# Kernel optimization log

Hardware: AMD Instinct MI355X
Metric: run time of the kernel (lower is better)

Reference implementation:

```python
import jax, jax.numpy as jnp
import numpy as np

# ---- static config (mirrors init_kwargs) ----
H, N, HKV = 32, 64, 8
HN = H * N            # model dim 2048
KV_DIM = HKV * N      # 512
B, T = 2, 1024
EPS = 1e-6
ROPE_THETA = 1.0e6
SPLITS_WAVGK = (96, 96, 64, 256, 64)   # xw, xa, xv, xg, xk lora ranks
SPLITS_RKV = (HN, KV_DIM, KV_DIM)


def rms_norm(x, w, eps=EPS):
    xf = x.astype(jnp.float32)
    var = jnp.mean(xf * xf, axis=-1, keepdims=True)
    return (w * (xf * jax.lax.rsqrt(var + eps))).astype(x.dtype)


def rotate_half(x):
    x1, x2 = jnp.split(x, 2, axis=-1)
    return jnp.concatenate((-x2, x1), axis=-1)


def apply_rope(q, k, cos, sin):
    # q:[B,T,H,N], k:[B,T,HKV,N], cos/sin:[B,T,N] -> unsqueeze head dim (unsqueeze_dim=2)
    cos = cos[:, :, None, :]
    sin = sin[:, :, None, :]
    return q * cos + rotate_half(q) * sin, k * cos + rotate_half(k) * sin


def rwkv7_recurrence(r, gk, k, v, a, b, S0):
    # fused_recurrent_rwkv7 (head_first=False). All inputs [B,T,H,N] fp32, S0 [B,H,N_key,N_val].
    # S_t = diag(exp(gk_t)) S_{t-1} + b_t (a_t^T S_{t-1}) + k_t v_t^T ;  o_t = r_t^T S_t
    def step(S, inp):
        r_t, w_t, k_t, v_t, a_t, b_t = inp
        sa = jnp.einsum('bhk,bhkv->bhv', a_t, S)
        S = (jnp.exp(w_t)[..., None] * S
             + k_t[..., None] * v_t[..., None, :]
             + b_t[..., None] * sa[..., None, :])
        o = jnp.einsum('bhk,bhkv->bhv', r_t, S)
        return S, o
    xs = tuple(jnp.swapaxes(t, 0, 1) for t in (r, gk, k, v, a, b))  # [T,B,H,N]
    S, o = jax.lax.scan(step, S0, xs)
    return jnp.swapaxes(o, 0, 1), S


def setup_inputs() -> dict:
    key = jax.random.key(0)
    ks = jax.random.split(key, 24)
    f32 = jnp.float32
    rn = lambda k, shape, s=1.0: jax.random.normal(k, shape, dtype=f32) * s

    x_in = rn(ks[0], (B, T, HN))
    v_first = rn(ks[1], (B, T, HKV, N))
    k_first = rn(ks[2], (B, T, HKV, N))
    state = jnp.zeros((B, H, N, N), f32)

    # real rope cache (faithful to get_batch_rope_cache output) at positions 0..T-1
    inv_freq = 1.0 / (ROPE_THETA ** (np.arange(0, N, 2, dtype=np.float32) / N))
    freqs = np.outer(np.arange(T, dtype=np.float32), inv_freq)  # [T, N/2]
    emb = np.concatenate([freqs, freqs], axis=-1)               # [T, N]
    calc_cos = jnp.broadcast_to(jnp.asarray(np.cos(emb), dtype=np.float32), (B, T, N))
    calc_sin = jnp.broadcast_to(jnp.asarray(np.sin(emb), dtype=np.float32), (B, T, N))

    wavgk1 = rn(ks[3], (HN, sum(SPLITS_WAVGK)), 0.02)
    w0 = rn(ks[4], (HN,), 0.5)
    w2 = rn(ks[5], (SPLITS_WAVGK[0], HN), 0.02)
    a0 = rn(ks[6], (HN,), 0.1)
    a2 = rn(ks[7], (SPLITS_WAVGK[1], HN), 0.02)
    v0 = rn(ks[8], (KV_DIM,), 0.1)
    v2 = rn(ks[9], (SPLITS_WAVGK[2], KV_DIM), 0.02)
    g2 = rn(ks[10], (SPLITS_WAVGK[3], HN), 0.02)
    k0 = rn(ks[11], (KV_DIM,), 0.1)
    k2 = rn(ks[12], (SPLITS_WAVGK[4], KV_DIM), 0.02)
    r_k = rn(ks[13], (H, N), 0.1)
    RKV = rn(ks[14], (HN, HN + 2 * KV_DIM), 0.02)   # fpx weight, dequantized form
    O = rn(ks[15], (HN, HN), 0.02)
    R_bias = rn(ks[16], (HN,), 0.02)
    K_bias = rn(ks[17], (KV_DIM,), 0.02)
    V_bias = rn(ks[18], (KV_DIM,), 0.02)
    ln_r = jnp.ones((N,), f32)
    ln_k = jnp.ones((N,), f32)
    ln1 = jnp.ones((HN,), f32)
    ln2 = jnp.ones((HN,), f32)

    return dict(x_in=x_in, v_first=v_first, k_first=k_first, state=state,
                calc_cos=calc_cos, calc_sin=calc_sin, wavgk1=wavgk1,
                w0=w0, w2=w2, a0=a0, a2=a2, v0=v0, v2=v2, g2=g2, k0=k0, k2=k2,
                r_k=r_k, RKV=RKV, O=O, R_bias=R_bias, K_bias=K_bias, V_bias=V_bias,
                ln_r=ln_r, ln_k=ln_k, ln1=ln1, ln2=ln2)


def reference(x_in, v_first, k_first, state, calc_cos, calc_sin, wavgk1,
              w0, w2, a0, a2, v0, v2, g2, k0, k2, r_k, RKV, O,
              R_bias, K_bias, V_bias, ln_r, ln_k, ln1, ln2):
    Bx, Tx, C = x_in.shape
    kv_repeat = HN // KV_DIM  # GQA repeat factor (4)

    x = rms_norm(x_in, ln1)
    xw, xa, xv, xg, xk = jnp.split(x @ wavgk1, np.cumsum(SPLITS_WAVGK)[:-1].tolist(), axis=-1)

    rkv = x @ RKV  # fpx_matmul -> dense matmul on dequantized weight
    r, k, v = jnp.split(rkv, np.cumsum(SPLITS_RKV)[:-1].tolist(), axis=-1)
    r = (r + R_bias).reshape(Bx, Tx, H, N)
    k = (k + K_bias).reshape(Bx, Tx, HKV, N)
    v = (v + V_bias).reshape(Bx, Tx, HKV, N)

    r = rms_norm(r, ln_r)
    k = rms_norm(k, ln_k)
    r, k = apply_rope(r, k, calc_cos, calc_sin)

    # layer_id = 1 (> 0): mix with first-layer value/key
    v = v + (v_first - v) * jax.nn.sigmoid(xv @ v2 + v0).reshape(Bx, Tx, HKV, N)
    k = k + (k_first - k) * jax.nn.sigmoid(xk @ k2 + k0).reshape(Bx, Tx, HKV, N)

    # repeat_kv: [B,T,HKV,N] -> [B,T,H,N] -> [B,T,HN]
    k = jnp.repeat(k, kv_repeat, axis=2).reshape(Bx, Tx, HN)
    v = jnp.repeat(v, kv_repeat, axis=2).reshape(Bx, Tx, HN)

    a = jax.nn.sigmoid(xa @ a2 + a0)  # in-context learning rate gate [B,T,HN]
    k4 = k.reshape(Bx, Tx, H, N)
    kk = (k4 / jnp.maximum(jnp.linalg.norm(k4, axis=-1, keepdims=True), 1e-12)).reshape(Bx, Tx, HN)

    w_log = -jax.nn.softplus(-(jnp.tanh(xw) @ w2 + w0)) - 0.5  # log-decay, <= -0.5
    k = k * (1.0 - w_log + a)
    aa = -kk
    bb = kk * a
    gk = -jnp.exp(w_log.astype(jnp.float32))  # passed to fused_recurrent_rwkv7 as log decay

    shp = (Bx, Tx, H, N)
    o, state_out = rwkv7_recurrence(
        r.reshape(shp).astype(jnp.float32), gk.reshape(shp),
        k.reshape(shp).astype(jnp.float32), v.reshape(shp).astype(jnp.float32),
        aa.reshape(shp).astype(jnp.float32), bb.reshape(shp).astype(jnp.float32),
        state.astype(jnp.float32))

    xx = o.reshape(Bx, Tx, HN) * (float(N) ** -0.5)
    bonus = ((r * k.reshape(shp) * r_k).sum(axis=-1, keepdims=True) * v.reshape(shp)).reshape(Bx, Tx, HN)
    xx = xx.astype(x_in.dtype) + bonus

    out = (xx * (jax.nn.sigmoid(xg) @ g2)) @ O  # fpx output projection
    x_new = x_in + out
    return rms_norm(x_new, ln2)
```

## Files before the change

kernel.cpp:

```cpp
#include <hip/hip_runtime.h>

typedef unsigned short u16;
typedef unsigned int u32;

using f32x4 = __attribute__((ext_vector_type(4))) float;
using bf16x8 = __attribute__((ext_vector_type(8))) __bf16;

#define HN 2048
#define KVD 512
#define TOKENS 2048
#define N1 3712
#define K2W 576
#define N2 7168

#define OFF_Y1   0ull
#define OFF_OO   0ull
#define OFF_XG   16777216ull
#define OFF_Y2   30408704ull
#define OFF_OUTR 60817408ull
#define OFF_BT1  89128960ull
#define OFF_XB   104333312ull
#define OFF_W2T  89128960ull
#define OFF_X2   97386496ull
#define OFF_OT   89128960ull
#define OFF_DEC  129499136ull
#define OFF_VV   163053568ull
#define OFF_PAB  213385216ull
#define OFF_PKR  230162432ull
#define OFF_DOT  246939648ull
#define WS_NEED  247201792ull

__device__ __forceinline__ u16 f2bf(float f) {
    u32 u = __float_as_uint(f);
    u32 r = u + 0x7fffu + ((u >> 16) & 1u);
    return (u16)(r >> 16);
}
__device__ __forceinline__ float bf2f(u16 b) {
    return __uint_as_float(((u32)b) << 16);
}
__device__ __forceinline__ float sigm(float x) { return 1.f / (1.f + expf(-x)); }
__device__ __forceinline__ float wsum(float v) {
#pragma unroll
    for (int m = 32; m > 0; m >>= 1) v += __shfl_xor(v, m, 64);
    return v;
}
__device__ __forceinline__ float rowsum16(float v) {
    float t;
    t = __uint_as_float(__builtin_amdgcn_update_dpp(0, __float_as_uint(v), 0x121, 0xf, 0xf, true));
    v += t;
    t = __uint_as_float(__builtin_amdgcn_update_dpp(0, __float_as_uint(v), 0x122, 0xf, 0xf, true));
    v += t;
    t = __uint_as_float(__builtin_amdgcn_update_dpp(0, __float_as_uint(v), 0x124, 0xf, 0xf, true));
    v += t;
    t = __uint_as_float(__builtin_amdgcn_update_dpp(0, __float_as_uint(v), 0x128, 0xf, 0xf, true));
    v += t;
    return v;
}

typedef __attribute__((address_space(1))) const void glob_t;
typedef __attribute__((address_space(3))) void lds_t;
__device__ __forceinline__ void gload_lds16(const void* g, void* l) {
    __builtin_amdgcn_global_load_lds((glob_t*)g, (lds_t*)l, 16, 0, 0);
}

template<int OFF>
__device__ __forceinline__ float4 ds_read128(u32 a) {
    float4 r;
    asm volatile("ds_read_b128 %0, %1 offset:%2" : "=v"(r) : "v"(a), "i"(OFF));
    return r;
}
template<int OFF>
__device__ __forceinline__ uint4 ds_read128u(u32 a) {
    uint4 r;
    asm volatile("ds_read_b128 %0, %1 offset:%2" : "=v"(r) : "v"(a), "i"(OFF));
    return r;
}
template<int OFF>
__device__ __forceinline__ float ds_read32(u32 a) {
    float r;
    asm volatile("ds_read_b32 %0, %1 offset:%2" : "=v"(r) : "v"(a), "i"(OFF));
    return r;
}

__global__ __launch_bounds__(256) void k_prep_bt1(const float* __restrict__ wavgk1,
                                                  const float* __restrict__ RKV,
                                                  u16* __restrict__ BT1) {
    __shared__ float tile[64][65];
    const int bn = blockIdx.x >> 5;
    const int bk = blockIdx.x & 31;
    const int n0 = bn << 6, k0 = bk << 6;
    const int c = threadIdx.x & 63, q = threadIdx.x >> 6;
#pragma unroll
    for (int i = 0; i < 16; ++i) {
        const int r = (q << 4) + i;
        float v = 0.f;
        if (bn < 9)       v = wavgk1[(size_t)(k0 + r) * 576 + n0 + c];
        else if (bn < 57) v = RKV[(size_t)(k0 + r) * 3072 + (n0 + c - 576)];
        tile[r][c] = v;
    }
    __syncthreads();
#pragma unroll
    for (int i = 0; i < 16; ++i) {
        const int rw = (q << 4) + i;
        BT1[(size_t)(n0 + rw) * 2048 + k0 + c] = f2bf(tile[c][rw]);
    }
}

__global__ __launch_bounds__(256) void k_prep_w2t(const float* __restrict__ w2, const float* __restrict__ a2,
                                                  const float* __restrict__ g2, const float* __restrict__ v2,
                                                  const float* __restrict__ k2, u16* __restrict__ W2T) {
    __shared__ float tile[64][65];
    const int bx = blockIdx.x;
    const int bn = bx / 9, bc = bx - bn * 9;
    const int n0 = bn << 6, c0 = bc << 6;
    const int cc = threadIdx.x & 63, q = threadIdx.x >> 6;
#pragma unroll
    for (int i = 0; i < 16; ++i) {
        const int r = (q << 4) + i;
        const int c = c0 + r;
        const int n = n0 + cc;
        float v = 0.f;
        if (n0 < 2048)      { if (c < 96)              v = w2[(size_t)c * 2048 + n]; }
        else if (n0 < 4096) { if (c >= 96 && c < 192)  v = a2[(size_t)(c - 96) * 2048 + (n - 2048)]; }
        else if (n0 < 6144) { if (c >= 192 && c < 448) v = g2[(size_t)(c - 192) * 2048 + (n - 4096)]; }
        else if (n0 < 6656) { if (c >= 448 && c < 512) v = v2[(size_t)(c - 448) * 512 + (n - 6144)]; }
        else                { if (c >= 512)            v = k2[(size_t)(c - 512) * 512 + (n - 6656)]; }
        tile[r][cc] = v;
    }
    __syncthreads();
#pragma unroll
    for (int i = 0; i < 16; ++i) {
        const int rw = (q << 4) + i;
        W2T[(size_t)(n0 + rw) * 576 + c0 + cc] = f2bf(tile[cc][rw]);
    }
}

__global__ __launch_bounds__(256) void k_prep_ot(const float* __restrict__ O, u16* __restrict__ OT) {
    __shared__ float tile[64][65];
    const int bn = blockIdx.x >> 5, bk = blockIdx.x & 31;
    const int n0 = bn << 6, k0 = bk << 6;
    const int c = threadIdx.x & 63, q = threadIdx.x >> 6;
#pragma unroll
    for (int i = 0; i < 16; ++i) {
        const int r = (q << 4) + i;
        tile[r][c] = O[(size_t)(k0 + r) * 2048 + n0 + c];
    }
    __syncthreads();
#pragma unroll
    for (int i = 0; i < 16; ++i) {
        const int rw = (q << 4) + i;
        OT[(size_t)(n0 + rw) * 2048 + k0 + c] = f2bf(tile[c][rw]);
    }
}

__global__ __launch_bounds__(256) void k_rms1(const float* __restrict__ X,
                                              const float* __restrict__ ln1,
                                              u16* __restrict__ XB) {
    const int t = blockIdx.x, tid = threadIdx.x;
    const float* row = X + ((size_t)t << 11);
    float4 v0 = *(const float4*)(row + tid * 8);
    float4 v1 = *(const float4*)(row + tid * 8 + 4);
    float ss = v0.x*v0.x + v0.y*v0.y + v0.z*v0.z + v0.w*v0.w
             + v1.x*v1.x + v1.y*v1.y + v1.z*v1.z + v1.w*v1.w;
    ss = wsum(ss);
    __shared__ float red[4];
    if ((tid & 63) == 0) red[tid >> 6] = ss;
    __syncthreads();
    float scale = rsqrtf((red[0] + red[1] + red[2] + red[3]) * (1.f / 2048.f) + 1e-6f);
    float4 w0_ = *(const float4*)(ln1 + tid * 8);
    float4 w1_ = *(const float4*)(ln1 + tid * 8 + 4);
    u16* o = XB + ((size_t)t << 11) + tid * 8;
    o[0] = f2bf(v0.x * scale * w0_.x); o[1] = f2bf(v0.y * scale * w0_.y);
    o[2] = f2bf(v0.z * scale * w0_.z); o[3] = f2bf(v0.w * scale * w0_.w);
    o[4] = f2bf(v1.x * scale * w1_.x); o[5] = f2bf(v1.y * scale * w1_.y);
    o[6] = f2bf(v1.z * scale * w1_.z); o[7] = f2bf(v1.w * scale * w1_.w);
}

__global__ __launch_bounds__(256) void k_gemm(const u16* __restrict__ A,
                                              const u16* __restrict__ Bt,
                                              float* __restrict__ C,
                                              int M, int N, int K) {
    __shared__ __align__(16) u16 tA[8192];
    __shared__ __align__(16) u16 tB[8192];
    const int tid = threadIdx.x;
    const int w = tid >> 6, l = tid & 63;
    const int bm = blockIdx.x << 7, bn = blockIdx.y << 7;
    const int wm = (w >> 1) << 6, wn = (w & 1) << 6;
    const int srow = (w << 3) + (l >> 3);
    const int lk = (((l & 7) ^ ((l >> 3) & 7)) << 3);
    const int frow = l & 15;
    f32x4 acc[4][4] = {};
    for (int kt = 0; kt < K; kt += 64) {
#pragma unroll
        for (int rr = 0; rr < 4; ++rr) {
            gload_lds16(A + (size_t)(bm + (rr << 5) + srow) * K + kt + lk,
                        &tA[(rr << 11) + (w << 9)]);
            gload_lds16(Bt + (size_t)(bn + (rr << 5) + srow) * K + kt + lk,
                        &tB[(rr << 11) + (w << 9)]);
        }
        __syncthreads();
#pragma unroll
        for (int s = 0; s < 2; ++s) {
            const int koff = ((((s << 2) + (l >> 4)) ^ (l & 7)) << 3);
            bf16x8 av[4], bv[4];
#pragma unroll
            for (int i = 0; i < 4; ++i) {
                av[i] = *(const bf16x8*)&tA[((wm + (i << 4) + frow) << 6) + koff];
                bv[i] = *(const bf16x8*)&tB[((wn + (i << 4) + frow) << 6) + koff];
            }
#pragma unroll
            for (int i = 0; i < 4; ++i)
#pragma unroll
                for (int j = 0; j < 4; ++j)
                    acc[i][j] = __builtin_amdgcn_mfma_f32_16x16x32_bf16(av[i], bv[j], acc[i][j], 0, 0, 0);
        }
        __syncthreads();
    }
    const int crow = bm + wm + ((l >> 4) << 2);
    const int ccol = bn + wn + (l & 15);
#pragma unroll
    for (int i = 0; i < 4; ++i)
#pragma unroll
        for (int j = 0; j < 4; ++j)
#pragma unroll
            for (int jj = 0; jj < 4; ++jj)
                C[(size_t)(crow + (i << 4) + jj) * N + ccol + (j << 4)] = acc[i][j][jj];
}

__global__ __launch_bounds__(256) void k_gemmb(const u16* __restrict__ A,
                                               const u16* __restrict__ Bt,
                                               u16* __restrict__ C,
                                               int M, int N, int K) {
    __shared__ __align__(16) u16 tA[8192];
    __shared__ __align__(16) u16 tB[8192];
    const int tid = threadIdx.x;
    const int w = tid >> 6, l = tid & 63;
    const int bm = blockIdx.x << 7, bn = blockIdx.y << 7;
    const int wm = (w >> 1) << 6, wn = (w & 1) << 6;
    const int srow = (w << 3) + (l >> 3);
    const int lk = (((l & 7) ^ ((l >> 3) & 7)) << 3);
    const int frow = l & 15;
    f32x4 acc[4][4] = {};
    for (int kt = 0; kt < K; kt += 64) {
#pragma unroll
        for (int rr = 0; rr < 4; ++rr) {
            gload_lds16(A + (size_t)(bm + (rr << 5) + srow) * K + kt + lk,
                        &tA[(rr << 11) + (w << 9)]);
            gload_lds16(Bt + (size_t)(bn + (rr << 5) + srow) * K + kt + lk,
                        &tB[(rr << 11) + (w << 9)]);
        }
        __syncthreads();
#pragma unroll
        for (int s = 0; s < 2; ++s) {
            const int koff = ((((s << 2) + (l >> 4)) ^ (l & 7)) << 3);
            bf16x8 av[4], bv[4];
#pragma unroll
            for (int i = 0; i < 4; ++i) {
                av[i] = *(const bf16x8*)&tA[((wm + (i << 4) + frow) << 6) + koff];
                bv[i] = *(const bf16x8*)&tB[((wn + (i << 4) + frow) << 6) + koff];
            }
#pragma unroll
            for (int i = 0; i < 4; ++i)
#pragma unroll
                for (int j = 0; j < 4; ++j)
                    acc[i][j] = __builtin_amdgcn_mfma_f32_16x16x32_bf16(av[i], bv[j], acc[i][j], 0, 0, 0);
        }
        __syncthreads();
    }
    const int crow = bm + wm + ((l >> 4) << 2);
    const int ccol = bn + wn + (l & 15);
#pragma unroll
    for (int i = 0; i < 4; ++i)
#pragma unroll
        for (int j = 0; j < 4; ++j)
#pragma unroll
            for (int jj = 0; jj < 4; ++jj)
                C[(size_t)(crow + (i << 4) + jj) * N + ccol + (j << 4)] = f2bf(acc[i][j][jj]);
}

__global__ __launch_bounds__(256) void k_gemm2(const u16* __restrict__ A,
                                               const u16* __restrict__ Bt,
                                               u16* __restrict__ C) {
    __shared__ __align__(16) u16 tA[4096];
    __shared__ __align__(16) u16 tB[4096];
    const int tid = threadIdx.x;
    const int w = tid >> 6, l = tid & 63;
    const int by = blockIdx.y;
    int c0, K;
    if (by < 16)      { c0 = 0;   K = 96; }
    else if (by < 32) { c0 = 96;  K = 96; }
    else if (by < 48) { c0 = 192; K = 256; }
    else if (by < 52) { c0 = 448; K = 64; }
    else              { c0 = 512; K = 64; }
    const int n0 = by << 7;
    const int bm = blockIdx.x << 7;
    const int wm = (w >> 1) << 6, wn = (w & 1) << 6;
    const int lrow = l >> 2;
    const int lk = (((l & 3) ^ ((l >> 3) & 3)) << 3);
    f32x4 acc[4][4] = {};
    const size_t rA0 = (size_t)(bm + (w << 4) + lrow) * 576 + c0;
    const size_t rA1 = (size_t)(bm + ((w + 4) << 4) + lrow) * 576 + c0;
    const size_t rB0 = (size_t)(n0 + (w << 4) + lrow) * 576 + c0;
    const size_t rB1 = (size_t)(n0 + ((w + 4) << 4) + lrow) * 576 + c0;
    const int frow = l & 15;
    const int koff = (((l >> 4) ^ ((l >> 1) & 3)) << 3);
    for (int kt = 0; kt < K; kt += 32) {
        gload_lds16(A + rA0 + kt + lk, &tA[w << 9]);
        gload_lds16(A + rA1 + kt + lk, &tA[2048 + (w << 9)]);
        gload_lds16(Bt + rB0 + kt + lk, &tB[w << 9]);
        gload_lds16(Bt + rB1 + kt + lk, &tB[2048 + (w << 9)]);
        __syncthreads();
        bf16x8 av[4], bv[4];
#pragma unroll
        for (int i = 0; i < 4; ++i) {
            av[i] = *(const bf16x8*)&tA[((wm + (i << 4) + frow) << 5) + koff];
            bv[i] = *(const bf16x8*)&tB[((wn + (i << 4) + frow) << 5) + koff];
        }
#pragma unroll
        for (int i = 0; i < 4; ++i)
#pragma unroll
            for (int j = 0; j < 4; ++j)
                acc[i][j] = __builtin_amdgcn_mfma_f32_16x16x32_bf16(av[i], bv[j], acc[i][j], 0, 0, 0);
        __syncthreads();
    }
    const int crow = bm + wm + ((l >> 4) << 2);
    const int ccol = n0 + wn + (l & 15);
#pragma unroll
    for (int i = 0; i < 4; ++i)
#pragma unroll
        for (int j = 0; j < 4; ++j)
#pragma unroll
            for (int jj = 0; jj < 4; ++jj)
                C[(size_t)(crow + (i << 4) + jj) * N2 + ccol + (j << 4)] = f2bf(acc[i][j][jj]);
}

__global__ __launch_bounds__(256) void k_prep_x2(const u16* __restrict__ Y1, u16* __restrict__ X2) {
    int idx = blockIdx.x * 256 + threadIdx.x;
    int t = idx / 576, c = idx - t * 576;
    const u16* y1 = Y1 + (size_t)t * N1;
    float v;
    if (c < 96)       v = tanhf(bf2f(y1[c]));
    else if (c < 192) v = bf2f(y1[c]);
    else if (c < 448) v = sigm(bf2f(y1[c + 64]));
    else if (c < 512) v = bf2f(y1[c - 256]);
    else              v = bf2f(y1[c]);
    X2[idx] = f2bf(v);
}

__global__ __launch_bounds__(256) void k_prep_rec(
    const u16* __restrict__ Y1, const u16* __restrict__ Y2b,
    const float* __restrict__ v_first, const float* __restrict__ k_first,
    const float* __restrict__ cosb, const float* __restrict__ sinb,
    const float* __restrict__ w0, const float* __restrict__ a0,
    const float* __restrict__ v0b, const float* __restrict__ k0b,
    const float* __restrict__ R_bias, const float* __restrict__ K_bias,
    const float* __restrict__ V_bias, const float* __restrict__ ln_r,
    const float* __restrict__ ln_k, const float* __restrict__ r_k,
    float* __restrict__ DEC, float* __restrict__ VV,
    u32* __restrict__ PAB, u32* __restrict__ PKR, float* __restrict__ DOT) {
    const int t = blockIdx.x, tid = threadIdx.x;
    const int ww = tid >> 6, lane = tid & 63;
    const u16* y1 = Y1 + (size_t)t * N1;
    const u16* y2 = Y2b + (size_t)t * N2;
    const float cs = cosb[t * 64 + lane];
    const float sn = sinb[t * 64 + lane];
    const float sign = lane < 32 ? -1.f : 1.f;
    const size_t tb = (size_t)t << 11;
    __shared__ float kkv[512], vkv[512];
    float rsave[8];
#pragma unroll
    for (int i = 0; i < 8; ++i) {
        int h = ww * 8 + i, c = h * 64 + lane;
        float rr = bf2f(y1[576 + c]) + R_bias[c];
        float ssq = wsum(rr * rr);
        float rn = ln_r[lane] * rr * rsqrtf(ssq * (1.f / 64.f) + 1e-6f);
        float rot = sign * __shfl(rn, lane ^ 32, 64);
        rsave[i] = rn * cs + rot * sn;
    }
#pragma unroll
    for (int i = 0; i < 2; ++i) {
        int j = ww * 2 + i, c = j * 64 + lane;
        float kr = bf2f(y1[2624 + c]) + K_bias[c];
        float ssq = wsum(kr * kr);
        float kn = ln_k[lane] * kr * rsqrtf(ssq * (1.f / 64.f) + 1e-6f);
        float rot = sign * __shfl(kn, lane ^ 32, 64);
        float krope = kn * cs + rot * sn;
        float ksig = sigm(bf2f(y2[6656 + c]) + k0b[c]);
        kkv[c] = krope + (k_first[(size_t)t * 512 + c] - krope) * ksig;
        float vr = bf2f(y1[3136 + c]) + V_bias[c];
        float vsig = sigm(bf2f(y2[6144 + c]) + v0b[c]);
        vkv[c] = vr + (v_first[(size_t)t * 512 + c] - vr) * vsig;
    }
    __syncthreads();
#pragma unroll
    for (int i = 0; i < 8; ++i) {
        int h = ww * 8 + i, c = h * 64 + lane;
        int ckv = (h >> 2) * 64 + lane;
        float kb = kkv[ckv], vb = vkv[ckv];
        float a_ = sigm(bf2f(y2[2048 + c]) + a0[c]);
        float wr = bf2f(y2[c]) + w0[c];
        float z = -wr;
        float sp = fmaxf(z, 0.f) + log1pf(expf(-fabsf(z)));
        float w_log = -sp - 0.5f;
        float ssq = wsum(kb * kb);
        float kk = kb / fmaxf(sqrtf(ssq), 1e-12f);
        const float kr2 = kb * (1.f - w_log + a_);
        const float rrv = rsave[i];
        DEC[tb + c] = expf(-expf(w_log));
        VV[tb + c] = vb;
        PAB[tb + c] = (u32)f2bf(-kk) | ((u32)f2bf(kk * a_) << 16);
        PKR[tb + c] = (u32)f2bf(kr2) | ((u32)f2bf(rrv) << 16);
        const float dsum = wsum(rrv * kr2 * r_k[c]);
        if (lane == 0) DOT[((size_t)t << 5) + h] = dsum;
    }
}

__global__ __launch_bounds__(256, 1) void k_recv17(
    const float* __restrict__ DECp, const u32* __restrict__ PABp,
    const u32* __restrict__ PKRp, const float* __restrict__ VVp,
    const float* __restrict__ S0, u16* __restrict__ OO) {
    __shared__ __align__(16) float cbuf[2][4][32][64];
    const int tid = threadIdx.x;
    const int wl = tid >> 6;
    const int lane = tid & 63;
    const int vl = lane >> 4;
    const int kq = lane & 15;
    const int quarter = blockIdx.x & 3;
    const int ch = blockIdx.x >> 2;
    const int vcol = (quarter << 4) + (wl << 2) + vl;
    const size_t cb = ((size_t)(ch >> 5) * 1024 * 2048) + ((size_t)(ch & 31) << 6);

    const float* s0 = S0 + ((size_t)ch << 12);
    float L0 = s0[((kq << 2) + 0) * 64 + vcol];
    float L1 = s0[((kq << 2) + 1) * 64 + vcol];
    float L2 = s0[((kq << 2) + 2) * 64 + vcol];
    float L3 = s0[((kq << 2) + 3) * 64 + vcol];

    const int trow = (wl << 2) + vl;

#define STG(B, T0)                                                             \
    {                                                                          \
        const size_t g0 = cb + (size_t)((T0) + trow) * 2048 + (kq << 2);       \
        const size_t g1 = cb + (size_t)((T0) + 16 + trow) * 2048 + (kq << 2);  \
        float* lb = &cbuf[B][0][0][0] + (wl << 8);                             \
        gload_lds16(DECp + g0, lb);                                            \
        gload_lds16(DECp + g1, lb + 1024);                                     \
        gload_lds16(PABp + g0, lb + 2048);                                     \
        gload_lds16(PABp + g1, lb + 3072);                                     \
        gload_lds16(PKRp + g0, lb + 4096);                                     \
        gload_lds16(PKRp + g1, lb + 5120);                                     \
        gload_lds16(VVp + g0, lb + 6144);                                      \
        gload_lds16(VVp + g1, lb + 7168);                                      \
    }

    const u32 base0 = (u32)(size_t)(void*)&cbuf[0][0][0][0];
    const u32 aA0 = base0 + (kq << 4);
    const u32 aV0 = base0 + 24576 + (vcol << 2);

    float4 cDa0, cDa1, cDb0, cDb1;
    uint4 cPAa0, cPAa1, cPAb0, cPAb1, cPKa0, cPKa1, cPKb0, cPKb1;
    float cV[32];

#define LD2(S_, G)                                                             \
    cD##S_##0 = ds_read128<(G) * 512>(aAb);                                    \
    cD##S_##1 = ds_read128<(G) * 512 + 256>(aAb);                              \
    cPA##S_##0 = ds_read128u<8192 + (G) * 512>(aAb);                           \
    cPA##S_##1 = ds_read128u<8192 + (G) * 512 + 256>(aAb);                     \
    cPK##S_##0 = ds_read128u<16384 + (G) * 512>(aAb);                          \
    cPK##S_##1 = ds_read128u<16384 + (G) * 512 + 256>(aAb);

#define VRD(J) cV[J] = ds_read32<(J) * 256>(aVb);
#define VRD8(J) VRD(J) VRD((J)+1) VRD((J)+2) VRD((J)+3) VRD((J)+4) VRD((J)+5) VRD((J)+6) VRD((J)+7)

#define WAIT6 asm volatile("s_waitcnt lgkmcnt(6)" ::: "memory");               \
    __builtin_amdgcn_sched_barrier(0);
#define WAIT0 asm volatile("s_waitcnt lgkmcnt(0)" ::: "memory");               \
    __builtin_amdgcn_sched_barrier(0);

#define UNP_LO(u) __uint_as_float((u) << 16)
#define UNP_HI(u) __uint_as_float((u) & 0xffff0000u)

#define STEP1(D4, pa, pk, Vsj, T)                                              \
    {                                                                          \
        const float Ax = UNP_LO(pa.x), Ay = UNP_LO(pa.y),                      \
                    Az = UNP_LO(pa.z), Aw = UNP_LO(pa.w);                      \
        const float Bx = UNP_HI(pa.x), By = UNP_HI(pa.y),                      \
                    Bz = UNP_HI(pa.z), Bw = UNP_HI(pa.w);                      \
        const float Kx = UNP_LO(pk.x), Ky = UNP_LO(pk.y),                      \
                    Kz = UNP_LO(pk.z), Kw = UNP_LO(pk.w);                      \
        const float Rx = UNP_HI(pk.x), Ry = UNP_HI(pk.y),                      \
                    Rz = UNP_HI(pk.z), Rw = UNP_HI(pk.w);                      \
        float sp = fmaf(L1, Ay, L0 * Ax) + fmaf(L3, Aw, L2 * Az);              \
        const float sa = rowsum16(sp);                                         \
        L0 = fmaf(Bx, sa, fmaf(Kx, Vsj, L0 * D4.x));                           \
        L1 = fmaf(By, sa, fmaf(Ky, Vsj, L1 * D4.y));                           \
        L2 = fmaf(Bz, sa, fmaf(Kz, Vsj, L2 * D4.z));                           \
        L3 = fmaf(Bw, sa, fmaf(Kw, Vsj, L3 * D4.w));                           \
        float op = fmaf(L1, Ry, L0 * Rx) + fmaf(L3, Rw, L2 * Rz);              \
        const float o = rowsum16(op);                                          \
        if (kq == 0) OO[cb + ((size_t)(T) << 11) + vcol] = f2bf(o);            \
    }

#define STEP2(S_, G)                                                           \
    STEP1(cD##S_##0, cPA##S_##0, cPK##S_##0, cV[2 * (G)], tbase + 2 * (G));    \
    STEP1(cD##S_##1, cPA##S_##1, cPK##S_##1, cV[2 * (G) + 1], tbase + 2 * (G) + 1);

#define PAIR(G)                                                                \
    LD2(b, (G) + 1) WAIT6 STEP2(a, G) LD2(a, (G) + 2) WAIT6 STEP2(b, (G) + 1)

    STG(0, 0);
    __syncthreads();

    for (int c = 0; c < 32; ++c) {
        const int b = c & 1;
        if (c < 31) STG(b ^ 1, (c + 1) << 5);
        const u32 aAb = aA0 + b * 32768;
        const u32 aVb = aV0 + b * 32768;
        const int tbase = c << 5;
        VRD8(0) VRD8(8) VRD8(16) VRD8(24)
        WAIT0
        LD2(a, 0)
        PAIR(0) PAIR(2) PAIR(4) PAIR(6) PAIR(8) PAIR(10) PAIR(12)
        LD2(b, 15) WAIT6 STEP2(a, 14) WAIT0 STEP2(b, 15)
        __syncthreads();
    }
#undef PAIR
#undef STEP2
#undef STEP1
#undef UNP_LO
#undef UNP_HI
#undef WAIT0
#undef WAIT6
#undef VRD8
#undef VRD
#undef LD2
#undef STG
}

__global__ __launch_bounds__(256) void k_gate(
    const u16* __restrict__ OOp, const float* __restrict__ VVp,
    const float* __restrict__ DOT, const u16* __restrict__ Y2b,
    u16* __restrict__ XG) {
    const int t = blockIdx.x, tid = threadIdx.x;
    const size_t tb = (size_t)t << 11;
    const int c0 = tid << 3;
    const float dot = DOT[((size_t)t << 5) + (tid >> 3)];
    uint4 ou = *(const uint4*)(OOp + tb + c0);
    float4 v0 = *(const float4*)(VVp + tb + c0);
    float4 v1 = *(const float4*)(VVp + tb + c0 + 4);
    uint4 gu = *(const uint4*)(Y2b + (size_t)t * N2 + 4096 + c0);
    const float o0 = __uint_as_float(ou.x << 16),  o1 = __uint_as_float(ou.x & 0xffff0000u);
    const float o2 = __uint_as_float(ou.y << 16),  o3 = __uint_as_float(ou.y & 0xffff0000u);
    const float o4 = __uint_as_float(ou.z << 16),  o5 = __uint_as_float(ou.z & 0xffff0000u);
    const float o6 = __uint_as_float(ou.w << 16),  o7 = __uint_as_float(ou.w & 0xffff0000u);
    const float g0 = __uint_as_float(gu.x << 16),  g1 = __uint_as_float(gu.x & 0xffff0000u);
    const float g2 = __uint_as_float(gu.y << 16),  g3 = __uint_as_float(gu.y & 0xffff0000u);
    const float g4 = __uint_as_float(gu.z << 16),  g5 = __uint_as_float(gu.z & 0xffff0000u);
    const float g6 = __uint_as_float(gu.w << 16),  g7 = __uint_as_float(gu.w & 0xffff0000u);
    const float x0 = fmaf(o0, 0.125f, dot * v0.x) * g0;
    const float x1 = fmaf(o1, 0.125f, dot * v0.y) * g1;
    const float x2 = fmaf(o2, 0.125f, dot * v0.z) * g2;
    const float x3 = fmaf(o3, 0.125f, dot * v0.w) * g3;
    const float x4 = fmaf(o4, 0.125f, dot * v1.x) * g4;
    const float x5 = fmaf(o5, 0.125f, dot * v1.y) * g5;
    const float x6 = fmaf(o6, 0.125f, dot * v1.z) * g6;
    const float x7 = fmaf(o7, 0.125f, dot * v1.w) * g7;
    uint4 pk;
    pk.x = (u32)f2bf(x0) | ((u32)f2bf(x1) << 16);
    pk.y = (u32)f2bf(x2) | ((u32)f2bf(x3) << 16);
    pk.z = (u32)f2bf(x4) | ((u32)f2bf(x5) << 16);
    pk.w = (u32)f2bf(x6) | ((u32)f2bf(x7) << 16);
    *(uint4*)(XG + tb + c0) = pk;
}

__global__ __launch_bounds__(256) void k_final(const float* __restrict__ x_in,
                                               const float* __restrict__ OUTR,
                                               const float* __restrict__ ln2,
                                               float* __restrict__ out) {
    const int t = blockIdx.x, tid = threadIdx.x;
    const float* xr = x_in + ((size_t)t << 11);
    const float* orow = OUTR + ((size_t)t << 11);
    float4 a0 = *(const float4*)(xr + tid * 8);
    float4 a1 = *(const float4*)(xr + tid * 8 + 4);
    float4 b0 = *(const float4*)(orow + tid * 8);
    float4 b1 = *(const float4*)(orow + tid * 8 + 4);
    float v[8] = {a0.x + b0.x, a0.y + b0.y, a0.z + b0.z, a0.w + b0.w,
                  a1.x + b1.x, a1.y + b1.y, a1.z + b1.z, a1.w + b1.w};
    float ss = 0.f;
#pragma unroll
    for (int i = 0; i < 8; ++i) ss = fmaf(v[i], v[i], ss);
    ss = wsum(ss);
    __shared__ float red[4];
    if ((tid & 63) == 0) red[tid >> 6] = ss;
    __syncthreads();
    float scale = rsqrtf((red[0] + red[1] + red[2] + red[3]) * (1.f / 2048.f) + 1e-6f);
    float* o = out + ((size_t)t << 11) + tid * 8;
#pragma unroll
    for (int i = 0; i < 8; ++i) o[i] = ln2[tid * 8 + i] * v[i] * scale;
}

extern "C" void kernel_launch(void* const* d_in, const int* in_sizes, int n_in,
                              void* d_out, int out_size, void* d_ws, size_t ws_size,
                              hipStream_t stream) {
    const float* x_in    = (const float*)d_in[0];
    const float* v_first = (const float*)d_in[1];
    const float* k_first = (const float*)d_in[2];
    const float* state   = (const float*)d_in[3];
    const float* cosb    = (const float*)d_in[4];
    const float* sinb    = (const float*)d_in[5];
    const float* wavgk1  = (const float*)d_in[6];
    const float* w0      = (const float*)d_in[7];
    const float* w2      = (const float*)d_in[8];
    const float* a0      = (const float*)d_in[9];
    const float* a2      = (const float*)d_in[10];
    const float* v0      = (const float*)d_in[11];
    const float* v2      = (const float*)d_in[12];
    const float* g2      = (const float*)d_in[13];
    const float* k0      = (const float*)d_in[14];
    const float* k2      = (const float*)d_in[15];
    const float* r_k     = (const float*)d_in[16];
    const float* RKV     = (const float*)d_in[17];
    const float* O       = (const float*)d_in[18];
    const float* R_bias  = (const float*)d_in[19];
    const float* K_bias  = (const float*)d_in[20];
    const float* V_bias  = (const float*)d_in[21];
    const float* ln_r    = (const float*)d_in[22];
    const float* ln_k    = (const float*)d_in[23];
    const float* ln1     = (const float*)d_in[24];
    const float* ln2     = (const float*)d_in[25];

    if (ws_size < WS_NEED) return;

    char* ws = (char*)d_ws;
    u16*   BT1  = (u16*)(ws + OFF_BT1);
    u16*   W2T  = (u16*)(ws + OFF_W2T);
    u16*   OT   = (u16*)(ws + OFF_OT);
    u16*   XB   = (u16*)(ws + OFF_XB);
    u16*   Y1   = (u16*)(ws + OFF_Y1);
    u16*   X2   = (u16*)(ws + OFF_X2);
    u16*   Y2b  = (u16*)(ws + OFF_Y2);
    float* DEC  = (float*)(ws + OFF_DEC);
    float* VV   = (float*)(ws + OFF_VV);
    u32*   PAB  = (u32*)(ws + OFF_PAB);
    u32*   PKR  = (u32*)(ws + OFF_PKR);
    float* DOT  = (float*)(ws + OFF_DOT);
    u16*   OO   = (u16*)(ws + OFF_OO);
    u16*   XG   = (u16*)(ws + OFF_XG);
    float* OUTR = (float*)(ws + OFF_OUTR);

    k_prep_bt1<<<1856, 256, 0, stream>>>(wavgk1, RKV, BT1);
    k_rms1<<<2048, 256, 0, stream>>>(x_in, ln1, XB);
    k_gemmb<<<dim3(16, 29), 256, 0, stream>>>(XB, BT1, Y1, 2048, N1, 2048);
    k_prep_w2t<<<1008, 256, 0, stream>>>(w2, a2, g2, v2, k2, W2T);
    k_prep_x2<<<4608, 256, 0, stream>>>(Y1, X2);
    k_gemm2<<<dim3(16, 56), 256, 0, stream>>>(X2, W2T, Y2b);
    k_prep_rec<<<2048, 256, 0, stream>>>(Y1, Y2b, v_first, k_first, cosb, sinb,
                                         w0, a0, v0, k0, R_bias, K_bias, V_bias,
                                         ln_r, ln_k, r_k, DEC, VV, PAB, PKR, DOT);
    k_prep_ot<<<1024, 256, 0, stream>>>(O, OT);
    k_recv17<<<256, 256, 0, stream>>>(DEC, PAB, PKR, VV, state, OO);
    k_gate<<<2048, 256, 0, stream>>>(OO, VV, DOT, Y2b, XG);
    k_gemm<<<dim3(16, 16), 256, 0, stream>>>(XG, OT, OUTR, 2048, 2048, 2048);
    k_final<<<2048, 256, 0, stream>>>(x_in, OUTR, ln2, (float*)d_out);
}
```

Measured before the change: 342.0 us.

## Merge prep kernels into one launch and fuse X2 activation into GEMM epilogue

Combines the four weight/activation prep kernels (BT1, W2T, OT transposes and RMSNorm) into a single block-indexed launch and rearranges workspace offsets so their outputs don't overlap. The tanh/sigmoid lora-input transform that built X2 moves into the first GEMM's epilogue, removing a separate pass over Y1. The recurrence output is now kept as fp32 instead of bf16, which removes a rounding step but doubles that buffer's traffic. Fewer launches and less intermediate memory traffic are the aim; the epilogue gains branches and scattered 2-byte stores.

```diff
diff --git a/kernel.cpp b/kernel.cpp
--- a/kernel.cpp
+++ b/kernel.cpp
@@ -16,13 +16,13 @@
 #define OFF_Y1   0ull
 #define OFF_OO   0ull
 #define OFF_XG   16777216ull
+#define OFF_W2T  16777216ull
+#define OFF_X2   25165824ull
 #define OFF_Y2   30408704ull
 #define OFF_OUTR 60817408ull
+#define OFF_OT   77594624ull
 #define OFF_BT1  89128960ull
 #define OFF_XB   104333312ull
-#define OFF_W2T  89128960ull
-#define OFF_X2   97386496ull
-#define OFF_OT   89128960ull
 #define OFF_DEC  129499136ull
 #define OFF_VV   163053568ull
 #define OFF_PAB  213385216ull
@@ -82,98 +82,94 @@
     return r;
 }
 
-__global__ __launch_bounds__(256) void k_prep_bt1(const float* __restrict__ wavgk1,
-                                                  const float* __restrict__ RKV,
-                                                  u16* __restrict__ BT1) {
-    __shared__ float tile[64][65];
-    const int bn = blockIdx.x >> 5;
-    const int bk = blockIdx.x & 31;
-    const int n0 = bn << 6, k0 = bk << 6;
-    const int c = threadIdx.x & 63, q = threadIdx.x >> 6;
-#pragma unroll
-    for (int i = 0; i < 16; ++i) {
-        const int r = (q << 4) + i;
-        float v = 0.f;
-        if (bn < 9)       v = wavgk1[(size_t)(k0 + r) * 576 + n0 + c];
-        else if (bn < 57) v = RKV[(size_t)(k0 + r) * 3072 + (n0 + c - 576)];
-        tile[r][c] = v;
-    }
-    __syncthreads();
-#pragma unroll
-    for (int i = 0; i < 16; ++i) {
-        const int rw = (q << 4) + i;
-        BT1[(size_t)(n0 + rw) * 2048 + k0 + c] = f2bf(tile[c][rw]);
-    }
-}
-
-__global__ __launch_bounds__(256) void k_prep_w2t(const float* __restrict__ w2, const float* __restrict__ a2,
-                                                  const float* __restrict__ g2, const float* __restrict__ v2,
-                                                  const float* __restrict__ k2, u16* __restrict__ W2T) {
+__global__ __launch_bounds__(256) void k_prep0(
+    const float* __restrict__ wavgk1, const float* __restrict__ RKV,
+    const float* __restrict__ w2, const float* __restrict__ a2,
+    const float* __restrict__ g2, const float* __restrict__ v2,
+    const float* __restrict__ k2, const float* __restrict__ O,
+    const float* __restrict__ X, const float* __restrict__ ln1,
+    u16* __restrict__ BT1, u16* __restrict__ W2T,
+    u16* __restrict__ OT, u16* __restrict__ XB) {
     __shared__ float tile[64][65];
     const int bx = blockIdx.x;
-    const int bn = bx / 9, bc = bx - bn * 9;
-    const int n0 = bn << 6, c0 = bc << 6;
-    const int cc = threadIdx.x & 63, q = threadIdx.x >> 6;
-#pragma unroll
-    for (int i = 0; i < 16; ++i) {
-        const int r = (q << 4) + i;
-        const int c = c0 + r;
-        const int n = n0 + cc;
-        float v = 0.f;
-        if (n0 < 2048)      { if (c < 96)              v = w2[(size_t)c * 2048 + n]; }
-        else if (n0 < 4096) { if (c >= 96 && c < 192)  v = a2[(size_t)(c - 96) * 2048 + (n - 2048)]; }
-        else if (n0 < 6144) { if (c >= 192 && c < 448) v = g2[(size_t)(c - 192) * 2048 + (n - 4096)]; }
-        else if (n0 < 6656) { if (c >= 448 && c < 512) v = v2[(size_t)(c - 448) * 512 + (n - 6144)]; }
-        else                { if (c >= 512)            v = k2[(size_t)(c - 512) * 512 + (n - 6656)]; }
-        tile[r][cc] = v;
-    }
-    __syncthreads();
-#pragma unroll
-    for (int i = 0; i < 16; ++i) {
-        const int rw = (q << 4) + i;
-        W2T[(size_t)(n0 + rw) * 576 + c0 + cc] = f2bf(tile[cc][rw]);
-    }
-}
-
-__global__ __launch_bounds__(256) void k_prep_ot(const float* __restrict__ O, u16* __restrict__ OT) {
-    __shared__ float tile[64][65];
-    const int bn = blockIdx.x >> 5, bk = blockIdx.x & 31;
-    const int n0 = bn << 6, k0 = bk << 6;
-    const int c = threadIdx.x & 63, q = threadIdx.x >> 6;
-#pragma unroll
-    for (int i = 0; i < 16; ++i) {
-        const int r = (q << 4) + i;
-        tile[r][c] = O[(size_t)(k0 + r) * 2048 + n0 + c];
-    }
-    __syncthreads();
-#pragma unroll
-    for (int i = 0; i < 16; ++i) {
-        const int rw = (q << 4) + i;
-        OT[(size_t)(n0 + rw) * 2048 + k0 + c] = f2bf(tile[c][rw]);
-    }
-}
-
-__global__ __launch_bounds__(256) void k_rms1(const float* __restrict__ X,
-                                              const float* __restrict__ ln1,
-                                              u16* __restrict__ XB) {
-    const int t = blockIdx.x, tid = threadIdx.x;
-    const float* row = X + ((size_t)t << 11);
-    float4 v0 = *(const float4*)(row + tid * 8);
-    float4 v1 = *(const float4*)(row + tid * 8 + 4);
-    float ss = v0.x*v0.x + v0.y*v0.y + v0.z*v0.z + v0.w*v0.w
-             + v1.x*v1.x + v1.y*v1.y + v1.z*v1.z + v1.w*v1.w;
-    ss = wsum(ss);
-    __shared__ float red[4];
-    if ((tid & 63) == 0) red[tid >> 6] = ss;
-    __syncthreads();
-    float scale = rsqrtf((red[0] + red[1] + red[2] + red[3]) * (1.f / 2048.f) + 1e-6f);
-    float4 w0_ = *(const float4*)(ln1 + tid * 8);
-    float4 w1_ = *(const float4*)(ln1 + tid * 8 + 4);
-    u16* o = XB + ((size_t)t << 11) + tid * 8;
-    o[0] = f2bf(v0.x * scale * w0_.x); o[1] = f2bf(v0.y * scale * w0_.y);
-    o[2] = f2bf(v0.z * scale * w0_.z); o[3] = f2bf(v0.w * scale * w0_.w);
-    o[4] = f2bf(v1.x * scale * w1_.x); o[5] = f2bf(v1.y * scale * w1_.y);
-    o[6] = f2bf(v1.z * scale * w1_.z); o[7] = f2bf(v1.w * scale * w1_.w);
+    const int tid = threadIdx.x;
+    if (bx < 1856) {
+        const int bn = bx >> 5, bk = bx & 31;
+        const int n0 = bn << 6, k0 = bk << 6;
+        const int c = tid & 63, q = tid >> 6;
+#pragma unroll
+        for (int i = 0; i < 16; ++i) {
+            const int r = (q << 4) + i;
+            float v = 0.f;
+            if (bn < 9)       v = wavgk1[(size_t)(k0 + r) * 576 + n0 + c];
+            else if (bn < 57) v = RKV[(size_t)(k0 + r) * 3072 + (n0 + c - 576)];
+            tile[r][c] = v;
+        }
+        __syncthreads();
+#pragma unroll
+        for (int i = 0; i < 16; ++i) {
+            const int rw = (q << 4) + i;
+            BT1[(size_t)(n0 + rw) * 2048 + k0 + c] = f2bf(tile[c][rw]);
+        }
+    } else if (bx < 2864) {
+        const int b = bx - 1856;
+        const int bn = b / 9, bc = b - bn * 9;
+        const int n0 = bn << 6, c0 = bc << 6;
+        const int cc = tid & 63, q = tid >> 6;
+#pragma unroll
+        for (int i = 0; i < 16; ++i) {
+            const int r = (q << 4) + i;
+            const int c = c0 + r;
+            const int n = n0 + cc;
+            float v = 0.f;
+            if (n0 < 2048)      { if (c < 96)              v = w2[(size_t)c * 2048 + n]; }
+            else if (n0 < 4096) { if (c >= 96 && c < 192)  v = a2[(size_t)(c - 96) * 2048 + (n - 2048)]; }
+            else if (n0 < 6144) { if (c >= 192 && c < 448) v = g2[(size_t)(c - 192) * 2048 + (n - 4096)]; }
+            else if (n0 < 6656) { if (c >= 448 && c < 512) v = v2[(size_t)(c - 448) * 512 + (n - 6144)]; }
+            else                { if (c >= 512)            v = k2[(size_t)(c - 512) * 512 + (n - 6656)]; }
+            tile[r][cc] = v;
+        }
+        __syncthreads();
+#pragma unroll
+        for (int i = 0; i < 16; ++i) {
+            const int rw = (q << 4) + i;
+            W2T[(size_t)(n0 + rw) * 576 + c0 + cc] = f2bf(tile[cc][rw]);
+        }
+    } else if (bx < 3888) {
+        const int b = bx - 2864;
+        const int bn = b >> 5, bk = b & 31;
+        const int n0 = bn << 6, k0 = bk << 6;
+        const int c = tid & 63, q = tid >> 6;
+#pragma unroll
+        for (int i = 0; i < 16; ++i) {
+            const int r = (q << 4) + i;
+            tile[r][c] = O[(size_t)(k0 + r) * 2048 + n0 + c];
+        }
+        __syncthreads();
+#pragma unroll
+        for (int i = 0; i < 16; ++i) {
+            const int rw = (q << 4) + i;
+            OT[(size_t)(n0 + rw) * 2048 + k0 + c] = f2bf(tile[c][rw]);
+        }
+    } else {
+        const int t = bx - 3888;
+        const float* row = X + ((size_t)t << 11);
+        float4 v0 = *(const float4*)(row + tid * 8);
+        float4 v1 = *(const float4*)(row + tid * 8 + 4);
+        float ss = v0.x*v0.x + v0.y*v0.y + v0.z*v0.z + v0.w*v0.w
+                 + v1.x*v1.x + v1.y*v1.y + v1.z*v1.z + v1.w*v1.w;
+        ss = wsum(ss);
+        if ((tid & 63) == 0) tile[0][tid >> 6] = ss;
+        __syncthreads();
+        float scale = rsqrtf((tile[0][0] + tile[0][1] + tile[0][2] + tile[0][3]) * (1.f / 2048.f) + 1e-6f);
+        float4 w0_ = *(const float4*)(ln1 + tid * 8);
+        float4 w1_ = *(const float4*)(ln1 + tid * 8 + 4);
+        u16* o = XB + ((size_t)t << 11) + tid * 8;
+        o[0] = f2bf(v0.x * scale * w0_.x); o[1] = f2bf(v0.y * scale * w0_.y);
+        o[2] = f2bf(v0.z * scale * w0_.z); o[3] = f2bf(v0.w * scale * w0_.w);
+        o[4] = f2bf(v1.x * scale * w1_.x); o[5] = f2bf(v1.y * scale * w1_.y);
+        o[6] = f2bf(v1.z * scale * w1_.z); o[7] = f2bf(v1.w * scale * w1_.w);
+    }
 }
 
 __global__ __launch_bounds__(256) void k_gemm(const u16* __restrict__ A,
@@ -230,6 +226,7 @@
 __global__ __launch_bounds__(256) void k_gemmb(const u16* __restrict__ A,
                                                const u16* __restrict__ Bt,
                                                u16* __restrict__ C,
+                                               u16* __restrict__ X2,
                                                int M, int N, int K) {
     __shared__ __align__(16) u16 tA[8192];
     __shared__ __align__(16) u16 tB[8192];
@@ -272,10 +269,24 @@
 #pragma unroll
     for (int i = 0; i < 4; ++i)
 #pragma unroll
-        for (int j = 0; j < 4; ++j)
-#pragma unroll
-            for (int jj = 0; jj < 4; ++jj)
-                C[(size_t)(crow + (i << 4) + jj) * N + ccol + (j << 4)] = f2bf(acc[i][j][jj]);
+        for (int j = 0; j < 4; ++j) {
+            const int c = ccol + (j << 4);
+#pragma unroll
+            for (int jj = 0; jj < 4; ++jj) {
+                const int t = crow + (i << 4) + jj;
+                const float y = acc[i][j][jj];
+                C[(size_t)t * N + c] = f2bf(y);
+                if (c < 576) {
+                    float v; int xc;
+                    if (c < 96)       { v = tanhf(y); xc = c; }
+                    else if (c < 192) { v = y;        xc = c; }
+                    else if (c < 256) { v = y;        xc = c + 256; }
+                    else if (c < 512) { v = sigm(y);  xc = c - 64; }
+                    else              { v = y;        xc = c; }
+                    X2[(size_t)t * 576 + xc] = f2bf(v);
+                }
+            }
+        }
 }
 
 __global__ __launch_bounds__(256) void k_gemm2(const u16* __restrict__ A,
@@ -334,19 +345,6 @@
                 C[(size_t)(crow + (i << 4) + jj) * N2 + ccol + (j << 4)] = f2bf(acc[i][j][jj]);
 }
 
-__global__ __launch_bounds__(256) void k_prep_x2(const u16* __restrict__ Y1, u16* __restrict__ X2) {
-    int idx = blockIdx.x * 256 + threadIdx.x;
-    int t = idx / 576, c = idx - t * 576;
-    const u16* y1 = Y1 + (size_t)t * N1;
-    float v;
-    if (c < 96)       v = tanhf(bf2f(y1[c]));
-    else if (c < 192) v = bf2f(y1[c]);
-    else if (c < 448) v = sigm(bf2f(y1[c + 64]));
-    else if (c < 512) v = bf2f(y1[c - 256]);
-    else              v = bf2f(y1[c]);
-    X2[idx] = f2bf(v);
-}
-
 __global__ __launch_bounds__(256) void k_prep_rec(
     const u16* __restrict__ Y1, const u16* __restrict__ Y2b,
     const float* __restrict__ v_first, const float* __restrict__ k_first,
@@ -418,7 +416,7 @@
 __global__ __launch_bounds__(256, 1) void k_recv17(
     const float* __restrict__ DECp, const u32* __restrict__ PABp,
     const u32* __restrict__ PKRp, const float* __restrict__ VVp,
-    const float* __restrict__ S0, u16* __restrict__ OO) {
+    const float* __restrict__ S0, float* __restrict__ OO) {
     __shared__ __align__(16) float cbuf[2][4][32][64];
     const int tid = threadIdx.x;
     const int wl = tid >> 6;
@@ -498,7 +496,7 @@
         L3 = fmaf(Bw, sa, fmaf(Kw, Vsj, L3 * D4.w));                           \
         float op = fmaf(L1, Ry, L0 * Rx) + fmaf(L3, Rw, L2 * Rz);              \
         const float o = rowsum16(op);                                          \
-        if (kq == 0) OO[cb + ((size_t)(T) << 11) + vcol] = f2bf(o);            \
+        if (kq == 0) OO[cb + ((size_t)(T) << 11) + vcol] = o;                  \
     }
 
 #define STEP2(S_, G)                                                           \
@@ -538,33 +536,30 @@
 }
 
 __global__ __launch_bounds__(256) void k_gate(
-    const u16* __restrict__ OOp, const float* __restrict__ VVp,
+    const float* __restrict__ OOp, const float* __restrict__ VVp,
     const float* __restrict__ DOT, const u16* __restrict__ Y2b,
     u16* __restrict__ XG) {
     const int t = blockIdx.x, tid = threadIdx.x;
     const size_t tb = (size_t)t << 11;
     const int c0 = tid << 3;
     const float dot = DOT[((size_t)t << 5) + (tid >> 3)];
-    uint4 ou = *(const uint4*)(OOp + tb + c0);
+    float4 o0 = *(const float4*)(OOp + tb + c0);
+    float4 o1 = *(const float4*)(OOp + tb + c0 + 4);
     float4 v0 = *(const float4*)(VVp + tb + c0);
     float4 v1 = *(const float4*)(VVp + tb + c0 + 4);
     uint4 gu = *(const uint4*)(Y2b + (size_t)t * N2 + 4096 + c0);
-    const float o0 = __uint_as_float(ou.x << 16),  o1 = __uint_as_float(ou.x & 0xffff0000u);
-    const float o2 = __uint_as_float(ou.y << 16),  o3 = __uint_as_float(ou.y & 0xffff0000u);
-    const float o4 = __uint_as_float(ou.z << 16),  o5 = __uint_as_float(ou.z & 0xffff0000u);
-    const float o6 = __uint_as_float(ou.w << 16),  o7 = __uint_as_float(ou.w & 0xffff0000u);
     const float g0 = __uint_as_float(gu.x << 16),  g1 = __uint_as_float(gu.x & 0xffff0000u);
     const float g2 = __uint_as_float(gu.y << 16),  g3 = __uint_as_float(gu.y & 0xffff0000u);
     const float g4 = __uint_as_float(gu.z << 16),  g5 = __uint_as_float(gu.z & 0xffff0000u);
     const float g6 = __uint_as_float(gu.w << 16),  g7 = __uint_as_float(gu.w & 0xffff0000u);
-    const float x0 = fmaf(o0, 0.125f, dot * v0.x) * g0;
-    const float x1 = fmaf(o1, 0.125f, dot * v0.y) * g1;
-    const float x2 = fmaf(o2, 0.125f, dot * v0.z) * g2;
-    const float x3 = fmaf(o3, 0.125f, dot * v0.w) * g3;
-    const float x4 = fmaf(o4, 0.125f, dot * v1.x) * g4;
-    const float x5 = fmaf(o5, 0.125f, dot * v1.y) * g5;
-    const float x6 = fmaf(o6, 0.125f, dot * v1.z) * g6;
-    const float x7 = fmaf(o7, 0.125f, dot * v1.w) * g7;
+    const float x0 = fmaf(o0.x, 0.125f, dot * v0.x) * g0;
+    const float x1 = fmaf(o0.y, 0.125f, dot * v0.y) * g1;
+    const float x2 = fmaf(o0.z, 0.125f, dot * v0.z) * g2;
+    const float x3 = fmaf(o0.w, 0.125f, dot * v0.w) * g3;
+    const float x4 = fmaf(o1.x, 0.125f, dot * v1.x) * g4;
+    const float x5 = fmaf(o1.y, 0.125f, dot * v1.y) * g5;
+    const float x6 = fmaf(o1.z, 0.125f, dot * v1.z) * g6;
+    const float x7 = fmaf(o1.w, 0.125f, dot * v1.w) * g7;
     uint4 pk;
     pk.x = (u32)f2bf(x0) | ((u32)f2bf(x1) << 16);
     pk.y = (u32)f2bf(x2) | ((u32)f2bf(x3) << 16);
@@ -644,20 +639,17 @@
     u32*   PAB  = (u32*)(ws + OFF_PAB);
     u32*   PKR  = (u32*)(ws + OFF_PKR);
     float* DOT  = (float*)(ws + OFF_DOT);
-    u16*   OO   = (u16*)(ws + OFF_OO);
+    float* OO   = (float*)(ws + OFF_OO);
     u16*   XG   = (u16*)(ws + OFF_XG);
     float* OUTR = (float*)(ws + OFF_OUTR);
 
-    k_prep_bt1<<<1856, 256, 0, stream>>>(wavgk1, RKV, BT1);
-    k_rms1<<<2048, 256, 0, stream>>>(x_in, ln1, XB);
-    k_gemmb<<<dim3(16, 29), 256, 0, stream>>>(XB, BT1, Y1, 2048, N1, 2048);
-    k_prep_w2t<<<1008, 256, 0, stream>>>(w2, a2, g2, v2, k2, W2T);
-    k_prep_x2<<<4608, 256, 0, stream>>>(Y1, X2);
+    k_prep0<<<5936, 256, 0, stream>>>(wavgk1, RKV, w2, a2, g2, v2, k2, O,
+                                      x_in, ln1, BT1, W2T, OT, XB);
+    k_gemmb<<<dim3(16, 29), 256, 0, stream>>>(XB, BT1, Y1, X2, 2048, N1, 2048);
     k_gemm2<<<dim3(16, 56), 256, 0, stream>>>(X2, W2T, Y2b);
     k_prep_rec<<<2048, 256, 0, stream>>>(Y1, Y2b, v_first, k_first, cosb, sinb,
                                          w0, a0, v0, k0, R_bias, K_bias, V_bias,
                                          ln_r, ln_k, r_k, DEC, VV, PAB, PKR, DOT);
-    k_prep_ot<<<1024, 256, 0, stream>>>(O, OT);
     k_recv17<<<256, 256, 0, stream>>>(DEC, PAB, PKR, VV, state, OO);
     k_gate<<<2048, 256, 0, stream>>>(OO, VV, DOT, Y2b, XG);
     k_gemm<<<dim3(16, 16), 256, 0, stream>>>(XG, OT, OUTR, 2048, 2048, 2048);
```

Result: no change. 339.7 us (-0.7%).
